# Optimization experiments

Hardware: AMD Instinct MI355X
Metric: run time of the kernel (lower is better)

The kernel has to match this reference:

```python
import jax, jax.numpy as jnp
import numpy as np

N, M, P = 8192, 8192, 16


def setup_inputs() -> dict:
    key = jax.random.key(0)
    k1, k2, k3, k4, k5 = jax.random.split(key, 5)
    x1 = jax.random.normal(k1, (N, P), dtype=jnp.float32)
    x2 = jax.random.normal(k2, (M, P), dtype=jnp.float32)
    # flax initializers.uniform() draws in [0, 0.01); use small scalars
    log_sigma_b = jax.random.uniform(k3, (), dtype=jnp.float32) * 0.01
    log_sigma_v = jax.random.uniform(k4, (), dtype=jnp.float32) * 0.01
    offset = jax.random.uniform(k5, (), dtype=jnp.float32) * 0.01
    return {"x1": x1, "x2": x2, "log_sigma_b": log_sigma_b,
            "log_sigma_v": log_sigma_v, "offset": offset}


def reference(x1, x2, log_sigma_b, log_sigma_v, offset):
    sigma_b = jnp.exp(log_sigma_b)
    sigma_v = jnp.exp(log_sigma_v)
    # sum_p (x1-offset)(x2-offset) as a dot product (n,p)@(p,m) -> (n,m)
    d = jnp.einsum("np,mp->nm", x1 - offset, x2 - offset)
    K = sigma_v ** 2 * d + sigma_b ** 2
    return K
```

## Files before the change

kernel.cpp:

```cpp
#include <hip/hip_runtime.h>
#include <cmath>


#define TILE 128
#define LDST 132

__global__ __launch_bounds__(256) void linear_kernel(
    const float* __restrict__ x1, const float* __restrict__ x2,
    const float* __restrict__ p_lsb, const float* __restrict__ p_lsv,
    const float* __restrict__ p_off, float* __restrict__ out, int ldout)
{
    __shared__ float s1[16 * LDST];
    __shared__ float s2[16 * LDST];

    const int tid = threadIdx.x;
    const int tx = tid & 15;
    const int ty = tid >> 4;
    const int n0 = blockIdx.y * TILE;
    const int m0 = blockIdx.x * TILE;

    const float off = p_off[0];
    const float sb  = expf(p_lsb[0]);
    const float sv  = expf(p_lsv[0]);
    const float sv2 = sv * sv;
    const float sb2 = sb * sb;

    const float4* g1 = (const float4*)(x1 + (size_t)n0 * 16);
    const float4* g2 = (const float4*)(x2 + (size_t)m0 * 16);
    #pragma unroll
    for (int j = tid; j < 512; j += 256) {
        const int row = j >> 2;
        const int p0  = (j & 3) * 4;
        float4 v = g1[j];
        s1[(p0 + 0) * LDST + row] = v.x - off;
        s1[(p0 + 1) * LDST + row] = v.y - off;
        s1[(p0 + 2) * LDST + row] = v.z - off;
        s1[(p0 + 3) * LDST + row] = v.w - off;
        float4 w = g2[j];
        s2[(p0 + 0) * LDST + row] = w.x - off;
        s2[(p0 + 1) * LDST + row] = w.y - off;
        s2[(p0 + 2) * LDST + row] = w.z - off;
        s2[(p0 + 3) * LDST + row] = w.w - off;
    }

    float acc[8][8];
    #pragma unroll
    for (int r = 0; r < 8; ++r)
        #pragma unroll
        for (int c = 0; c < 8; ++c) acc[r][c] = 0.0f;

    __syncthreads();

    #pragma unroll
    for (int p = 0; p < 16; ++p) {
        const float* s1p = &s1[p * LDST];
        const float* s2p = &s2[p * LDST];
        const float4 a0 = *(const float4*)&s1p[ty * 4];
        const float4 a1 = *(const float4*)&s1p[64 + ty * 4];
        const float4 b0 = *(const float4*)&s2p[tx * 4];
        const float4 b1 = *(const float4*)&s2p[64 + tx * 4];
        const float av[8] = {a0.x, a0.y, a0.z, a0.w, a1.x, a1.y, a1.z, a1.w};
        const float bv[8] = {b0.x, b0.y, b0.z, b0.w, b1.x, b1.y, b1.z, b1.w};
        #pragma unroll
        for (int r = 0; r < 8; ++r)
            #pragma unroll
            for (int c = 0; c < 8; ++c)
                acc[r][c] += av[r] * bv[c];
    }

    #pragma unroll
    for (int r = 0; r < 8; ++r) {
        const int lr  = (r < 4) ? (ty * 4 + r) : (64 + ty * 4 + (r - 4));
        float* orow = out + (size_t)(n0 + lr) * (size_t)ldout + m0;
        float4 o0, o1;
        o0.x = sv2 * acc[r][0] + sb2;
        o0.y = sv2 * acc[r][1] + sb2;
        o0.z = sv2 * acc[r][2] + sb2;
        o0.w = sv2 * acc[r][3] + sb2;
        o1.x = sv2 * acc[r][4] + sb2;
        o1.y = sv2 * acc[r][5] + sb2;
        o1.z = sv2 * acc[r][6] + sb2;
        o1.w = sv2 * acc[r][7] + sb2;
        *(float4*)&orow[tx * 4]      = o0;
        *(float4*)&orow[64 + tx * 4] = o1;
    }
}

extern "C" void kernel_launch(void* const* d_in, const int* in_sizes, int n_in,
                              void* d_out, int out_size, void* d_ws, size_t ws_size,
                              hipStream_t stream) {
    const float* x1  = (const float*)d_in[0];
    const float* x2  = (const float*)d_in[1];
    const float* lsb = (const float*)d_in[2];
    const float* lsv = (const float*)d_in[3];
    const float* off = (const float*)d_in[4];
    float* out = (float*)d_out;

    const int n = in_sizes[0] / 16;
    const int m = in_sizes[1] / 16;

    dim3 grid(m / TILE, n / TILE);
    linear_kernel<<<grid, 256, 0, stream>>>(x1, x2, lsb, lsv, off, out, m);
}
```

Before: 273.5 us.

## Replace shared-memory tiled GEMM with register-resident column strip streaming rows

After: 291.3 us. +6.5%, slower.

```diff
diff --git a/kernel.cpp b/kernel.cpp
--- a/kernel.cpp
+++ b/kernel.cpp
@@ -2,87 +2,75 @@
 #include <cmath>
 
 
-#define TILE 128
-#define LDST 132
+typedef float f32x4 __attribute__((ext_vector_type(4)));
 
-__global__ __launch_bounds__(256) void linear_kernel(
+#define ROWS_PER_BLOCK 32
+#define BLOCK_COLS 1024
+
+__global__ __launch_bounds__(256, 4) void linear_kernel(
     const float* __restrict__ x1, const float* __restrict__ x2,
     const float* __restrict__ p_lsb, const float* __restrict__ p_lsv,
-    const float* __restrict__ p_off, float* __restrict__ out, int ldout)
+    const float* __restrict__ p_off, float* __restrict__ out,
+    int n, int m)
 {
-    __shared__ float s1[16 * LDST];
-    __shared__ float s2[16 * LDST];
-
-    const int tid = threadIdx.x;
-    const int tx = tid & 15;
-    const int ty = tid >> 4;
-    const int n0 = blockIdx.y * TILE;
-    const int m0 = blockIdx.x * TILE;
+    const int lane = threadIdx.x & 63;
+    const int wid  = __builtin_amdgcn_readfirstlane(threadIdx.x >> 6);
+    const int c0   = blockIdx.x * BLOCK_COLS + wid * 256 + (lane << 2);
+    const int n0   = blockIdx.y * ROWS_PER_BLOCK;
 
     const float off = p_off[0];
+    const float sv  = expf(p_lsv[0]);
     const float sb  = expf(p_lsb[0]);
-    const float sv  = expf(p_lsv[0]);
     const float sv2 = sv * sv;
     const float sb2 = sb * sb;
 
-    const float4* g1 = (const float4*)(x1 + (size_t)n0 * 16);
-    const float4* g2 = (const float4*)(x2 + (size_t)m0 * 16);
+    float C[4][16];
+    float bias[4];
     #pragma unroll
-    for (int j = tid; j < 512; j += 256) {
-        const int row = j >> 2;
-        const int p0  = (j & 3) * 4;
-        float4 v = g1[j];
-        s1[(p0 + 0) * LDST + row] = v.x - off;
-        s1[(p0 + 1) * LDST + row] = v.y - off;
-        s1[(p0 + 2) * LDST + row] = v.z - off;
-        s1[(p0 + 3) * LDST + row] = v.w - off;
-        float4 w = g2[j];
-        s2[(p0 + 0) * LDST + row] = w.x - off;
-        s2[(p0 + 1) * LDST + row] = w.y - off;
-        s2[(p0 + 2) * LDST + row] = w.z - off;
-        s2[(p0 + 3) * LDST + row] = w.w - off;
+    for (int c = 0; c < 4; ++c) {
+        const f32x4* g = (const f32x4*)(x2 + (size_t)(c0 + c) * 16);
+        float s = 0.0f;
+        #pragma unroll
+        for (int q = 0; q < 4; ++q) {
+            f32x4 v = g[q];
+            #pragma unroll
+            for (int j = 0; j < 4; ++j) {
+                const float t = sv2 * (v[j] - off);
+                C[c][q * 4 + j] = t;
+                s += t;
+            }
+        }
+        bias[c] = sb2 - off * s;
     }
 
-    float acc[8][8];
-    #pragma unroll
-    for (int r = 0; r < 8; ++r)
+    float* orow = out + (size_t)n0 * m + c0;
+    const f32x4* arow = (const f32x4*)(x1 + (size_t)n0 * 16);
+    #pragma unroll 2
+    for (int r = 0; r < ROWS_PER_BLOCK; ++r) {
+        const f32x4 a0 = arow[0];
+        const f32x4 a1 = arow[1];
+        const f32x4 a2 = arow[2];
+        const f32x4 a3 = arow[3];
+        float a[16];
         #pragma unroll
-        for (int c = 0; c < 8; ++c) acc[r][c] = 0.0f;
-
-    __syncthreads();
-
-    #pragma unroll
-    for (int p = 0; p < 16; ++p) {
-        const float* s1p = &s1[p * LDST];
-        const float* s2p = &s2[p * LDST];
-        const float4 a0 = *(const float4*)&s1p[ty * 4];
-        const float4 a1 = *(const float4*)&s1p[64 + ty * 4];
-        const float4 b0 = *(const float4*)&s2p[tx * 4];
-        const float4 b1 = *(const float4*)&s2p[64 + tx * 4];
-        const float av[8] = {a0.x, a0.y, a0.z, a0.w, a1.x, a1.y, a1.z, a1.w};
-        const float bv[8] = {b0.x, b0.y, b0.z, b0.w, b1.x, b1.y, b1.z, b1.w};
+        for (int j = 0; j < 4; ++j) {
+            a[j]      = a0[j];
+            a[4 + j]  = a1[j];
+            a[8 + j]  = a2[j];
+            a[12 + j] = a3[j];
+        }
+        f32x4 acc;
+        acc[0] = bias[0]; acc[1] = bias[1]; acc[2] = bias[2]; acc[3] = bias[3];
         #pragma unroll
-        for (int r = 0; r < 8; ++r)
-            #pragma unroll
-            for (int c = 0; c < 8; ++c)
-                acc[r][c] += av[r] * bv[c];
-    }
-
-    #pragma unroll
-    for (int r = 0; r < 8; ++r) {
-        const int lr  = (r < 4) ? (ty * 4 + r) : (64 + ty * 4 + (r - 4));
-        float* orow = out + (size_t)(n0 + lr) * (size_t)ldout + m0;
-        float4 o0, o1;
-        o0.x = sv2 * acc[r][0] + sb2;
-        o0.y = sv2 * acc[r][1] + sb2;
-        o0.z = sv2 * acc[r][2] + sb2;
-        o0.w = sv2 * acc[r][3] + sb2;
-        o1.x = sv2 * acc[r][4] + sb2;
-        o1.y = sv2 * acc[r][5] + sb2;
-        o1.z = sv2 * acc[r][6] + sb2;
-        o1.w = sv2 * acc[r][7] + sb2;
-        *(float4*)&orow[tx * 4]      = o0;
-        *(float4*)&orow[64 + tx * 4] = o1;
+        for (int p = 0; p < 16; ++p) {
+            acc[0] = fmaf(a[p], C[0][p], acc[0]);
+            acc[1] = fmaf(a[p], C[1][p], acc[1]);
+            acc[2] = fmaf(a[p], C[2][p], acc[2]);
+            acc[3] = fmaf(a[p], C[3][p], acc[3]);
+        }
+        *(f32x4*)orow = acc;
+        orow += m;
+        arow += 4;
     }
 }
 
@@ -99,6 +87,6 @@
     const int n = in_sizes[0] / 16;
     const int m = in_sizes[1] / 16;
 
-    dim3 grid(m / TILE, n / TILE);
-    linear_kernel<<<grid, 256, 0, stream>>>(x1, x2, lsb, lsv, off, out, m);
+    dim3 grid(m / BLOCK_COLS, n / ROWS_PER_BLOCK);
+    linear_kernel<<<grid, 256, 0, stream>>>(x1, x2, lsb, lsv, off, out, n, m);
 }
```
